# Optimization experiments

Hardware: AMD Instinct MI355X
Metric: run time of the kernel (lower is better)

## Reference

```python
import jax, jax.numpy as jnp
import numpy as np

H_DIM = 1024
N_HEADS = 16
HEAD_D = H_DIM // N_HEADS  # 64


def setup_inputs() -> dict:
    key = jax.random.key(0)
    ks = jax.random.split(key, 10)
    B, T, C = 2, 2048, H_DIM
    init = 1.0 / np.sqrt(C)  # lecun_normal-scale stand-in
    src = jax.random.normal(ks[0], (B, T, C), dtype=jnp.float32)
    mask = jnp.ones((B, T), dtype=jnp.float32)  # unused when causal
    Wq = jax.random.normal(ks[1], (C, H_DIM), dtype=jnp.float32) * init
    Wk = jax.random.normal(ks[2], (C, H_DIM), dtype=jnp.float32) * init
    Wv = jax.random.normal(ks[3], (C, H_DIM), dtype=jnp.float32) * init
    Wo = jax.random.normal(ks[4], (H_DIM, H_DIM), dtype=jnp.float32) * init
    bq = jnp.zeros((H_DIM,), jnp.float32)
    bk = jnp.zeros((H_DIM,), jnp.float32)
    bv = jnp.zeros((H_DIM,), jnp.float32)
    bo = jnp.zeros((H_DIM,), jnp.float32)
    return {"src": src, "mask": mask, "Wq": Wq, "bq": bq, "Wk": Wk, "bk": bk,
            "Wv": Wv, "bv": bv, "Wo": Wo, "bo": bo}


def reference(src, mask, Wq, bq, Wk, bk, Wv, bv, Wo, bo):
    # MaskedCausalAttention forward, deterministic=True (dropout = identity),
    # use_causal_mask=True.
    B, T, C = src.shape
    N, D = N_HEADS, HEAD_D
    # q,k,v: [B, N, T, D]
    q = (src @ Wq + bq).reshape(B, T, N, D).transpose(0, 2, 1, 3)
    k = (src @ Wk + bk).reshape(B, T, N, D).transpose(0, 2, 1, 3)
    v = (src @ Wv + bv).reshape(B, T, N, D).transpose(0, 2, 1, 3)
    # scores: [B, N, T, T]
    scores = jnp.einsum('bntd,bnsd->bnts', q, k) / jnp.sqrt(jnp.float32(D))
    causal = jnp.tril(jnp.ones((T, T), dtype=bool))[None, None]
    scores = jnp.where(causal, scores, -jnp.inf)
    probs = jax.nn.softmax(scores, axis=-1)
    attn = jnp.einsum('bnts,bnsd->bntd', probs, v)  # [B, N, T, D]
    attn = attn.transpose(0, 2, 1, 3).reshape(B, T, N * D)
    return attn @ Wo + bo
```

## Files before the change

### kernel.cpp

```cpp
#include <hip/hip_runtime.h>
#include <hip/hip_bf16.h>

typedef __hip_bfloat16 bf16;
typedef __attribute__((ext_vector_type(8))) short short8;
typedef __attribute__((ext_vector_type(4))) float f32x4;

#define BATCH 2
#define SEQ   2048
#define HDIM  1024
#define NHEAD 16
#define DHEAD 64
#define MROWS (BATCH*SEQ)

#define QSCALE 0.18033688f
#define EXP2F(x) __builtin_amdgcn_exp2f(x)

static __device__ __forceinline__ short f2bs(float x) {
    __hip_bfloat16 h = (__hip_bfloat16)x;
    return *reinterpret_cast<short*>(&h);
}
static __device__ __forceinline__ unsigned int pk2(float a, float b) {
    __hip_bfloat162 h = __float22bfloat162_rn(make_float2(a, b));
    return *reinterpret_cast<unsigned int*>(&h);
}

static __device__ __forceinline__ void gload16(const void* g, void* l) {
    __builtin_amdgcn_global_load_lds(
        (const __attribute__((address_space(1))) unsigned int*)g,
        (__attribute__((address_space(3))) unsigned int*)l, 16, 0, 0);
}

__global__ __launch_bounds__(256) void prep1(const float* __restrict__ src,
        const float* __restrict__ Wq, const float* __restrict__ Wk,
        const float* __restrict__ Wv,
        short* __restrict__ Sb, short* __restrict__ WqkT,
        short* __restrict__ WvT)
{
    __shared__ float t[64][65];
    const int bx = blockIdx.x, tid = threadIdx.x;
    if (bx < 4096) {
        int i = bx * 256 + tid;
        float4 v = ((const float4*)src)[i];
        ushort4 o;
        o.x = (unsigned short)f2bs(v.x);
        o.y = (unsigned short)f2bs(v.y);
        o.z = (unsigned short)f2bs(v.z);
        o.w = (unsigned short)f2bs(v.w);
        ((ushort4*)Sb)[i] = o;
        return;
    }
    const int tb = bx - 4096;
    const int wsel = tb >> 8;
    const float* W = (wsel == 0) ? Wq : (wsel == 1) ? Wk : Wv;
    short* dst = (wsel < 2) ? WqkT : WvT;
    const int roff = (wsel < 2) ? wsel * 1024 : 0;
    const int t8 = tb & 255;
    const int n0 = (t8 & 15) * 64, k0 = (t8 >> 4) * 64;
#pragma unroll
    for (int i = 0; i < 16; i++) {
        int idx = tid + i * 256, r = idx >> 6, c = idx & 63;
        t[r][c] = W[(size_t)(k0 + r) * HDIM + n0 + c];
    }
    __syncthreads();
#pragma unroll
    for (int i = 0; i < 16; i++) {
        int idx = tid + i * 256, c = idx >> 6, r = idx & 63;
        dst[(size_t)(roff + n0 + c) * HDIM + k0 + r] = f2bs(t[r][c]);
    }
}

__global__ __launch_bounds__(256) void gemm_qk(const short* __restrict__ A,
        const short* __restrict__ Bt,
        const float* __restrict__ bq, const float* __restrict__ bk,
        short* __restrict__ Qout, short* __restrict__ Kout)
{
    __shared__ short As[2][4 * 512];
    __shared__ short Bs[2][8 * 512];
    const int tid = threadIdx.x, lane = tid & 63, w = tid >> 6;
    const int quad = lane >> 4, l15 = lane & 15;
    const int m0 = blockIdx.y * 64, n0 = blockIdx.x * 128;
    const int wr = w >> 1, wc = w & 1;

    const short* gsrc[3];
    short* dst0[3];
    short* dst1[3];
#pragma unroll
    for (int i = 0; i < 3; i++) {
        int u = w * 3 + i;
        if (u < 4) {
            gsrc[i] = A + (size_t)(m0 + u * 16 + l15) * HDIM + quad * 8;
            dst0[i] = &As[0][u * 512];
            dst1[i] = &As[1][u * 512];
        } else {
            int c = u - 4;
            gsrc[i] = Bt + (size_t)(n0 + c * 16 + l15) * HDIM + quad * 8;
            dst0[i] = &Bs[0][c * 512];
            dst1[i] = &Bs[1][c * 512];
        }
    }

    f32x4 acc[2][4];
#pragma unroll
    for (int i = 0; i < 2; i++)
#pragma unroll
        for (int j = 0; j < 4; j++) acc[i][j] = (f32x4){0.f, 0.f, 0.f, 0.f};

#pragma unroll
    for (int i = 0; i < 3; i++) { gload16(gsrc[i], dst0[i]); gsrc[i] += 32; }
    __syncthreads();

    for (int kk = 0; kk < 32; ++kk) {
        const int cur = kk & 1;
        if (kk < 31) {
#pragma unroll
            for (int i = 0; i < 3; i++) {
                gload16(gsrc[i], cur ? dst0[i] : dst1[i]);
                gsrc[i] += 32;
            }
        }
        short8 af[2], bfr[4];
#pragma unroll
        for (int mi = 0; mi < 2; mi++)
            af[mi] = *(const short8*)&As[cur][(wr * 2 + mi) * 512 + lane * 8];
#pragma unroll
        for (int ni = 0; ni < 4; ni++)
            bfr[ni] = *(const short8*)&Bs[cur][(wc * 4 + ni) * 512 + lane * 8];
#pragma unroll
        for (int mi = 0; mi < 2; mi++)
#pragma unroll
            for (int ni = 0; ni < 4; ni++)
                acc[mi][ni] = __builtin_amdgcn_mfma_f32_16x16x32_bf16(
                                  af[mi], bfr[ni], acc[mi][ni], 0, 0, 0);
        __syncthreads();
    }

    const int region = n0 >> 10;
    const float* bias = region ? bk : bq;
    const float oscale = region ? 1.0f : QSCALE;
    short* C = region ? Kout : Qout;

#pragma unroll
    for (int mi = 0; mi < 2; mi++) {
        int mB = m0 + (wr * 2 + mi) * 16 + quad * 4;
#pragma unroll
        for (int ni = 0; ni < 4; ni++) {
            int nl = (n0 + (wc * 4 + ni) * 16 + l15) & 1023;
            float bb = bias[nl];
#pragma unroll
            for (int r = 0; r < 4; r++)
                C[(size_t)(mB + r) * HDIM + nl] =
                    f2bs((acc[mi][ni][r] + bb) * oscale);
        }
    }
}

__global__ __launch_bounds__(256) void gemm_v(const short* __restrict__ A,
        const short* __restrict__ Bt, const float* __restrict__ bv,
        short* __restrict__ Vtout)
{
    __shared__ short As[2][4 * 512];
    __shared__ short Bs[2][8 * 512];
    const int tid = threadIdx.x, lane = tid & 63, w = tid >> 6;
    const int quad = lane >> 4, l15 = lane & 15;
    const int m0 = blockIdx.y * 64, n0 = blockIdx.x * 128;
    const int wr = w >> 1, wc = w & 1;

    const short* gsrc[3];
    short* dst0[3];
    short* dst1[3];
#pragma unroll
    for (int i = 0; i < 3; i++) {
        int u = w * 3 + i;
        if (u < 4) {
            gsrc[i] = A + (size_t)(m0 + u * 16 + l15) * HDIM + quad * 8;
            dst0[i] = &As[0][u * 512];
            dst1[i] = &As[1][u * 512];
        } else {
            int c = u - 4;
            gsrc[i] = Bt + (size_t)(n0 + c * 16 + l15) * HDIM + quad * 8;
            dst0[i] = &Bs[0][c * 512];
            dst1[i] = &Bs[1][c * 512];
        }
    }

    f32x4 acc[2][4];
#pragma unroll
    for (int i = 0; i < 2; i++)
#pragma unroll
        for (int j = 0; j < 4; j++) acc[i][j] = (f32x4){0.f, 0.f, 0.f, 0.f};

#pragma unroll
    for (int i = 0; i < 3; i++) { gload16(gsrc[i], dst0[i]); gsrc[i] += 32; }
    __syncthreads();

    for (int kk = 0; kk < 32; ++kk) {
        const int cur = kk & 1;
        if (kk < 31) {
#pragma unroll
            for (int i = 0; i < 3; i++) {
                gload16(gsrc[i], cur ? dst0[i] : dst1[i]);
                gsrc[i] += 32;
            }
        }
        short8 af[2], bfr[4];
#pragma unroll
        for (int mi = 0; mi < 2; mi++)
            af[mi] = *(const short8*)&As[cur][(wr * 2 + mi) * 512 + lane * 8];
#pragma unroll
        for (int ni = 0; ni < 4; ni++)
            bfr[ni] = *(const short8*)&Bs[cur][(wc * 4 + ni) * 512 + lane * 8];
#pragma unroll
        for (int mi = 0; mi < 2; mi++)
#pragma unroll
            for (int ni = 0; ni < 4; ni++)
                acc[mi][ni] = __builtin_amdgcn_mfma_f32_16x16x32_bf16(
                                  af[mi], bfr[ni], acc[mi][ni], 0, 0, 0);
        __syncthreads();
    }

#pragma unroll
    for (int mi = 0; mi < 2; mi++) {
        int mB = m0 + (wr * 2 + mi) * 16 + quad * 4;
        int bb = mB >> 11, t = mB & 2047;
#pragma unroll
        for (int ni = 0; ni < 4; ni++) {
            int n = n0 + (wc * 4 + ni) * 16 + l15;
            int h = n >> 6, d = n & 63;
            float bvv = bv[n];
            size_t base = ((size_t)((bb * NHEAD + h) * DHEAD + d)) * SEQ + t;
            ushort4 pk;
            pk.x = (unsigned short)f2bs(acc[mi][ni][0] + bvv);
            pk.y = (unsigned short)f2bs(acc[mi][ni][1] + bvv);
            pk.z = (unsigned short)f2bs(acc[mi][ni][2] + bvv);
            pk.w = (unsigned short)f2bs(acc[mi][ni][3] + bvv);
            *(ushort4*)(Vtout + base) = pk;
        }
    }
}

__global__ __launch_bounds__(256) void gemm_o(const short* __restrict__ A,
        const short* __restrict__ Bt, const float* __restrict__ bo,
        float* __restrict__ Out)
{
    __shared__ short As[2][4 * 512];
    __shared__ short Bs[2][8 * 512];
    const int tid = threadIdx.x, lane = tid & 63, w = tid >> 6;
    const int quad = lane >> 4, l15 = lane & 15;
    const int m0 = blockIdx.y * 64, n0 = blockIdx.x * 128;
    const int wr = w >> 1, wc = w & 1;

    const short* gsrc[3];
    short* dst0[3];
    short* dst1[3];
#pragma unroll
    for (int i = 0; i < 3; i++) {
        int u = w * 3 + i;
        if (u < 4) {
            gsrc[i] = A + (size_t)(m0 + u * 16 + l15) * HDIM + quad * 8;
            dst0[i] = &As[0][u * 512];
            dst1[i] = &As[1][u * 512];
        } else {
            int c = u - 4;
            gsrc[i] = Bt + (size_t)(n0 + c * 16 + l15) * HDIM + quad * 8;
            dst0[i] = &Bs[0][c * 512];
            dst1[i] = &Bs[1][c * 512];
        }
    }

    f32x4 acc[2][4];
#pragma unroll
    for (int i = 0; i < 2; i++)
#pragma unroll
        for (int j = 0; j < 4; j++) acc[i][j] = (f32x4){0.f, 0.f, 0.f, 0.f};

#pragma unroll
    for (int i = 0; i < 3; i++) { gload16(gsrc[i], dst0[i]); gsrc[i] += 32; }
    __syncthreads();

    for (int kk = 0; kk < 32; ++kk) {
        const int cur = kk & 1;
        if (kk < 31) {
#pragma unroll
            for (int i = 0; i < 3; i++) {
                gload16(gsrc[i], cur ? dst0[i] : dst1[i]);
                gsrc[i] += 32;
            }
        }
        short8 af[2], bfr[4];
#pragma unroll
        for (int mi = 0; mi < 2; mi++)
            af[mi] = *(const short8*)&As[cur][(wr * 2 + mi) * 512 + lane * 8];
#pragma unroll
        for (int ni = 0; ni < 4; ni++)
            bfr[ni] = *(const short8*)&Bs[cur][(wc * 4 + ni) * 512 + lane * 8];
#pragma unroll
        for (int mi = 0; mi < 2; mi++)
#pragma unroll
            for (int ni = 0; ni < 4; ni++)
                acc[mi][ni] = __builtin_amdgcn_mfma_f32_16x16x32_bf16(
                                  af[mi], bfr[ni], acc[mi][ni], 0, 0, 0);
        __syncthreads();
    }

#pragma unroll
    for (int mi = 0; mi < 2; mi++) {
        int mB = m0 + (wr * 2 + mi) * 16 + quad * 4;
#pragma unroll
        for (int ni = 0; ni < 4; ni++) {
            int n = n0 + (wc * 4 + ni) * 16 + l15;
            float bb = bo[n];
#pragma unroll
            for (int r = 0; r < 4; r++)
                Out[(size_t)(mB + r) * HDIM + n] = acc[mi][ni][r] + bb;
        }
    }
}

__global__ __launch_bounds__(256) void attn_mfma(const short* __restrict__ Qb,
        const short* __restrict__ Kb, const short* __restrict__ Vt,
        short* __restrict__ Ab,
        const float* __restrict__ Wo, short* __restrict__ WoT)
{
    __shared__ short SMEM[12800];
    short* Ks = SMEM;
    short* Vs = SMEM + 4096;
    short* Ps = SMEM + 8192;
    const int tid = threadIdx.x, lane = tid & 63, w = tid >> 6;
    const int quad = lane >> 4, l15 = lane & 15;
    const int L = blockIdx.x;

    if (L >= 1024) {
        float* t = (float*)SMEM;
        const int bsel = L - 1024;
#pragma unroll
        for (int j = 0; j < 8; j++) {
            int t8 = bsel * 8 + j;
            int n0 = (t8 & 15) * 64, k0 = (t8 >> 4) * 64;
            __syncthreads();
#pragma unroll
            for (int i = 0; i < 16; i++) {
                int idx = tid + i * 256, r = idx >> 6, c = idx & 63;
                t[r * 65 + c] = Wo[(size_t)(k0 + r) * HDIM + n0 + c];
            }
            __syncthreads();
#pragma unroll
            for (int i = 0; i < 16; i++) {
                int idx = tid + i * 256, c = idx >> 6, r = idx & 63;
                WoT[(size_t)(n0 + c) * HDIM + k0 + r] = f2bs(t[r * 65 + c]);
            }
        }
        return;
    }

    const int pair = (L & 7) + 8 * ((L >> 3) & 3);
    const int strip = 31 - (L >> 5);
    const int b = pair >> 4, head = pair & 15;

    const short* Kbh = Kb + (size_t)b * SEQ * HDIM + head * DHEAD;
    const short* Vth = Vt + (size_t)(b * NHEAD + head) * DHEAD * SEQ;
    short* Pw = &Ps[w * 1152];

    const int qbase = strip * 64;
    const int qr = qbase + w * 16 + l15;

    const short* qptr = Qb + (size_t)(b * SEQ + qr) * HDIM + head * DHEAD + quad * 8;
    short8 bq0 = *(const short8*)qptr;
    short8 bq1 = *(const short8*)(qptr + 32);

    f32x4 o[4];
#pragma unroll
    for (int dt = 0; dt < 4; dt++) o[dt] = (f32x4){0.f, 0.f, 0.f, 0.f};
    float psum = 0.f;

    for (int it = 0; it <= strip; ++it) {
        const int s0 = it * 64;
#pragma unroll
        for (int i = 0; i < 4; i++) {
            int u = w * 4 + i;
            if (u < 8) {
                int t = u >> 1, h = u & 1;
                gload16(Kbh + (size_t)(s0 + t * 16 + l15) * HDIM + h * 32 + quad * 8,
                        &Ks[u * 512]);
            } else {
                int c = u - 8, dt = c >> 1, kh = c & 1;
                gload16(Vth + (size_t)(dt * 16 + l15) * SEQ + s0 + kh * 32 + quad * 8,
                        &Vs[c * 512]);
            }
        }
        __syncthreads();

        f32x4 sv[4];
#pragma unroll
        for (int t = 0; t < 4; t++) {
            sv[t] = (f32x4){0.f, 0.f, 0.f, 0.f};
            short8 k0 = *(const short8*)&Ks[(t * 2) * 512 + lane * 8];
            short8 k1 = *(const short8*)&Ks[(t * 2 + 1) * 512 + lane * 8];
            sv[t] = __builtin_amdgcn_mfma_f32_16x16x32_bf16(k0, bq0, sv[t], 0, 0, 0);
            sv[t] = __builtin_amdgcn_mfma_f32_16x16x32_bf16(k1, bq1, sv[t], 0, 0, 0);
        }

        float p[16];
        if (it == strip) {
#pragma unroll
            for (int t = 0; t < 4; t++)
#pragma unroll
                for (int r = 0; r < 4; r++) {
                    int key = s0 + t * 16 + quad * 4 + r;
                    p[t * 4 + r] = (key <= qr) ? EXP2F(sv[t][r]) : 0.f;
                }
        } else {
#pragma unroll
            for (int t = 0; t < 4; t++)
#pragma unroll
                for (int r = 0; r < 4; r++)
                    p[t * 4 + r] = EXP2F(sv[t][r]);
        }
#pragma unroll
        for (int i = 0; i < 16; i++) psum += p[i];

#pragma unroll
        for (int t = 0; t < 4; t++) {
            uint2 u2;
            u2.x = pk2(p[t * 4],     p[t * 4 + 1]);
            u2.y = pk2(p[t * 4 + 2], p[t * 4 + 3]);
            *(uint2*)&Pw[l15 * 72 + t * 16 + quad * 4] = u2;
        }
        short8 bp0 = *(const short8*)&Pw[l15 * 72 + quad * 8];
        short8 bp1 = *(const short8*)&Pw[l15 * 72 + 32 + quad * 8];

#pragma unroll
        for (int dt = 0; dt < 4; dt++) {
            short8 av0 = *(const short8*)&Vs[(dt * 2) * 512 + lane * 8];
            short8 av1 = *(const short8*)&Vs[(dt * 2 + 1) * 512 + lane * 8];
            o[dt] = __builtin_amdgcn_mfma_f32_16x16x32_bf16(av0, bp0, o[dt], 0, 0, 0);
            o[dt] = __builtin_amdgcn_mfma_f32_16x16x32_bf16(av1, bp1, o[dt], 0, 0, 0);
        }
        __syncthreads();
    }

    float lrow = psum + __shfl_xor(psum, 16);
    lrow += __shfl_xor(lrow, 32);
    const float inv = 1.f / lrow;

    const size_t obase = (size_t)(b * SEQ + qr) * HDIM + head * DHEAD;
#pragma unroll
    for (int dt = 0; dt < 4; dt++) {
        uint2 u2;
        u2.x = pk2(o[dt][0] * inv, o[dt][1] * inv);
        u2.y = pk2(o[dt][2] * inv, o[dt][3] * inv);
        *(uint2*)&Ab[obase + dt * 16 + quad * 4] = u2;
    }
}

extern "C" void kernel_launch(void* const* d_in, const int* in_sizes, int n_in,
                              void* d_out, int out_size, void* d_ws, size_t ws_size,
                              hipStream_t stream)
{
    const float* src = (const float*)d_in[0];
    const float* Wq = (const float*)d_in[2];
    const float* bq = (const float*)d_in[3];
    const float* Wk = (const float*)d_in[4];
    const float* bk = (const float*)d_in[5];
    const float* Wv = (const float*)d_in[6];
    const float* bv = (const float*)d_in[7];
    const float* Wo = (const float*)d_in[8];
    const float* bo = (const float*)d_in[9];
    float* out = (float*)d_out;

    short* Sb   = (short*)d_ws;
    short* Qb   = Sb + (size_t)MROWS * HDIM;
    short* Kb   = Qb + (size_t)MROWS * HDIM;
    short* Vt   = Kb + (size_t)MROWS * HDIM;
    short* slot = Vt + (size_t)MROWS * HDIM;
    short* WqkT = Vt;
    short* Ab   = Qb;

    dim3 blk(256);

    prep1<<<dim3(4096 + 768), blk, 0, stream>>>(src, Wq, Wk, Wv, Sb, WqkT, slot);

    gemm_qk<<<dim3(16, 64), blk, 0, stream>>>(Sb, WqkT, bq, bk, Qb, Kb);

    gemm_v<<<dim3(8, 64), blk, 0, stream>>>(Sb, slot, bv, Vt);

    attn_mfma<<<dim3(1024 + 32), blk, 0, stream>>>(Qb, Kb, Vt, Ab, Wo, slot);

    gemm_o<<<dim3(8, 64), blk, 0, stream>>>(Ab, slot, bo, out);
}
```

Measured before the change: 240.3 us.

## Fuse src bf16 conversion into a single QKV GEMM and move Wo transpose to prep

Removes the separate pass that converts src to bf16 and instead loads fp32 src directly in the GEMM, converting in registers before the LDS store. Merges the QK and V projection GEMMs into one launch over a 3072-wide concatenated weight with a larger 128x128 tile, and moves the Wo transpose out of the attention kernel into the weight prep kernel. This cuts a full read/write round trip of the activation and one launch, at the cost of more registers per thread (16 accumulators) and synchronous fp32 global loads in the GEMM loop.

Result: slower. 247.4 us (+3.0%).

```diff
diff --git a/kernel.cpp b/kernel.cpp
--- a/kernel.cpp
+++ b/kernel.cpp
@@ -30,31 +30,19 @@
         (__attribute__((address_space(3))) unsigned int*)l, 16, 0, 0);
 }
 
-__global__ __launch_bounds__(256) void prep1(const float* __restrict__ src,
-        const float* __restrict__ Wq, const float* __restrict__ Wk,
-        const float* __restrict__ Wv,
-        short* __restrict__ Sb, short* __restrict__ WqkT,
-        short* __restrict__ WvT)
+__global__ __launch_bounds__(256) void prep(const float* __restrict__ Wq,
+        const float* __restrict__ Wk, const float* __restrict__ Wv,
+        const float* __restrict__ Wo,
+        short* __restrict__ WqkvT, short* __restrict__ WoT)
 {
     __shared__ float t[64][65];
-    const int bx = blockIdx.x, tid = threadIdx.x;
-    if (bx < 4096) {
-        int i = bx * 256 + tid;
-        float4 v = ((const float4*)src)[i];
-        ushort4 o;
-        o.x = (unsigned short)f2bs(v.x);
-        o.y = (unsigned short)f2bs(v.y);
-        o.z = (unsigned short)f2bs(v.z);
-        o.w = (unsigned short)f2bs(v.w);
-        ((ushort4*)Sb)[i] = o;
-        return;
-    }
-    const int tb = bx - 4096;
-    const int wsel = tb >> 8;
-    const float* W = (wsel == 0) ? Wq : (wsel == 1) ? Wk : Wv;
-    short* dst = (wsel < 2) ? WqkT : WvT;
-    const int roff = (wsel < 2) ? wsel * 1024 : 0;
-    const int t8 = tb & 255;
+    const int tid = threadIdx.x;
+    const int wsel = blockIdx.x >> 8;
+    const float* W = (wsel == 0) ? Wq : (wsel == 1) ? Wk
+                    : (wsel == 2) ? Wv : Wo;
+    short* dst = (wsel < 3) ? WqkvT : WoT;
+    const int roff = (wsel < 3) ? wsel * 1024 : 0;
+    const int t8 = blockIdx.x & 255;
     const int n0 = (t8 & 15) * 64, k0 = (t8 >> 4) * 64;
 #pragma unroll
     for (int i = 0; i < 16; i++) {
@@ -69,10 +57,154 @@
     }
 }
 
-__global__ __launch_bounds__(256) void gemm_qk(const short* __restrict__ A,
+__global__ __launch_bounds__(256) void gemm_qkv(const float* __restrict__ src,
         const short* __restrict__ Bt,
         const float* __restrict__ bq, const float* __restrict__ bk,
-        short* __restrict__ Qout, short* __restrict__ Kout)
+        const float* __restrict__ bv,
+        short* __restrict__ Qout, short* __restrict__ Kout,
+        short* __restrict__ Vtout)
+{
+    __shared__ short As[2][8 * 512];
+    __shared__ short Bs[2][8 * 512];
+    const int tid = threadIdx.x, lane = tid & 63, w = tid >> 6;
+    const int quad = lane >> 4, l15 = lane & 15;
+    const int m0 = blockIdx.y * 128, n0 = blockIdx.x * 128;
+    const int wr = w >> 1, wc = w & 1;
+
+    const float* ag[2];
+    short* adst0[2];
+    short* adst1[2];
+#pragma unroll
+    for (int c = 0; c < 2; c++) {
+        int u = 2 * w + c;
+        ag[c] = src + (size_t)(m0 + u * 16 + l15) * HDIM + quad * 8;
+        adst0[c] = &As[0][u * 512 + lane * 8];
+        adst1[c] = &As[1][u * 512 + lane * 8];
+    }
+    const short* bg[2];
+    short* bdst0[2];
+    short* bdst1[2];
+#pragma unroll
+    for (int c = 0; c < 2; c++) {
+        int u = 2 * w + c;
+        bg[c] = Bt + (size_t)(n0 + u * 16 + l15) * HDIM + quad * 8;
+        bdst0[c] = &Bs[0][u * 512];
+        bdst1[c] = &Bs[1][u * 512];
+    }
+
+    f32x4 acc[4][4];
+#pragma unroll
+    for (int i = 0; i < 4; i++)
+#pragma unroll
+        for (int j = 0; j < 4; j++) acc[i][j] = (f32x4){0.f, 0.f, 0.f, 0.f};
+
+    {
+        float4 a4[2][2];
+#pragma unroll
+        for (int c = 0; c < 2; c++) {
+            a4[c][0] = *(const float4*)(ag[c]);
+            a4[c][1] = *(const float4*)(ag[c] + 4);
+            ag[c] += 32;
+            gload16(bg[c], bdst0[c]);
+            bg[c] += 32;
+        }
+#pragma unroll
+        for (int c = 0; c < 2; c++) {
+            uint4 u;
+            u.x = pk2(a4[c][0].x, a4[c][0].y);
+            u.y = pk2(a4[c][0].z, a4[c][0].w);
+            u.z = pk2(a4[c][1].x, a4[c][1].y);
+            u.w = pk2(a4[c][1].z, a4[c][1].w);
+            *(uint4*)adst0[c] = u;
+        }
+    }
+    __syncthreads();
+
+    for (int kk = 0; kk < 32; ++kk) {
+        const int cur = kk & 1;
+        float4 a4[2][2];
+        if (kk < 31) {
+#pragma unroll
+            for (int c = 0; c < 2; c++) {
+                a4[c][0] = *(const float4*)(ag[c]);
+                a4[c][1] = *(const float4*)(ag[c] + 4);
+                ag[c] += 32;
+                gload16(bg[c], cur ? bdst0[c] : bdst1[c]);
+                bg[c] += 32;
+            }
+        }
+
+        short8 af[4], bfr[4];
+#pragma unroll
+        for (int mi = 0; mi < 4; mi++)
+            af[mi] = *(const short8*)&As[cur][(wr * 4 + mi) * 512 + lane * 8];
+#pragma unroll
+        for (int ni = 0; ni < 4; ni++)
+            bfr[ni] = *(const short8*)&Bs[cur][(wc * 4 + ni) * 512 + lane * 8];
+#pragma unroll
+        for (int mi = 0; mi < 4; mi++)
+#pragma unroll
+            for (int ni = 0; ni < 4; ni++)
+                acc[mi][ni] = __builtin_amdgcn_mfma_f32_16x16x32_bf16(
+                                  af[mi], bfr[ni], acc[mi][ni], 0, 0, 0);
+
+        if (kk < 31) {
+#pragma unroll
+            for (int c = 0; c < 2; c++) {
+                uint4 u;
+                u.x = pk2(a4[c][0].x, a4[c][0].y);
+                u.y = pk2(a4[c][0].z, a4[c][0].w);
+                u.z = pk2(a4[c][1].x, a4[c][1].y);
+                u.w = pk2(a4[c][1].z, a4[c][1].w);
+                *(uint4*)(cur ? adst0[c] : adst1[c]) = u;
+            }
+        }
+        __syncthreads();
+    }
+
+    const int region = n0 >> 10;
+    const float* bias = (region == 0) ? bq : (region == 1) ? bk : bv;
+    const float oscale = (region == 0) ? QSCALE : 1.0f;
+
+    float bvv[4];
+    int nl4[4];
+#pragma unroll
+    for (int ni = 0; ni < 4; ni++) {
+        int n = n0 + (wc * 4 + ni) * 16 + l15;
+        nl4[ni] = n & 1023;
+        bvv[ni] = bias[nl4[ni]];
+    }
+
+#pragma unroll
+    for (int mi = 0; mi < 4; mi++) {
+        int mB = m0 + (wr * 4 + mi) * 16 + quad * 4;
+#pragma unroll
+        for (int ni = 0; ni < 4; ni++) {
+            int nl = nl4[ni];
+            if (region == 2) {
+                int bb = mB >> 11, t = mB & 2047;
+                int h = nl >> 6, d = nl & 63;
+                size_t base = ((size_t)((bb * NHEAD + h) * DHEAD + d)) * SEQ + t;
+                ushort4 pk;
+                pk.x = (unsigned short)f2bs(acc[mi][ni][0] + bvv[ni]);
+                pk.y = (unsigned short)f2bs(acc[mi][ni][1] + bvv[ni]);
+                pk.z = (unsigned short)f2bs(acc[mi][ni][2] + bvv[ni]);
+                pk.w = (unsigned short)f2bs(acc[mi][ni][3] + bvv[ni]);
+                *(ushort4*)(Vtout + base) = pk;
+            } else {
+                short* C = (region == 0) ? Qout : Kout;
+#pragma unroll
+                for (int r = 0; r < 4; r++)
+                    C[(size_t)(mB + r) * HDIM + nl] =
+                        f2bs((acc[mi][ni][r] + bvv[ni]) * oscale);
+            }
+        }
+    }
+}
+
+__global__ __launch_bounds__(256) void gemm_o(const short* __restrict__ A,
+        const short* __restrict__ Bt, const float* __restrict__ bo,
+        float* __restrict__ Out)
 {
     __shared__ short As[2][4 * 512];
     __shared__ short Bs[2][8 * 512];
@@ -134,174 +266,6 @@
         __syncthreads();
     }
 
-    const int region = n0 >> 10;
-    const float* bias = region ? bk : bq;
-    const float oscale = region ? 1.0f : QSCALE;
-    short* C = region ? Kout : Qout;
-
-#pragma unroll
-    for (int mi = 0; mi < 2; mi++) {
-        int mB = m0 + (wr * 2 + mi) * 16 + quad * 4;
-#pragma unroll
-        for (int ni = 0; ni < 4; ni++) {
-            int nl = (n0 + (wc * 4 + ni) * 16 + l15) & 1023;
-            float bb = bias[nl];
-#pragma unroll
-            for (int r = 0; r < 4; r++)
-                C[(size_t)(mB + r) * HDIM + nl] =
-                    f2bs((acc[mi][ni][r] + bb) * oscale);
-        }
-    }
-}
-
-__global__ __launch_bounds__(256) void gemm_v(const short* __restrict__ A,
-        const short* __restrict__ Bt, const float* __restrict__ bv,
-        short* __restrict__ Vtout)
-{
-    __shared__ short As[2][4 * 512];
-    __shared__ short Bs[2][8 * 512];
-    const int tid = threadIdx.x, lane = tid & 63, w = tid >> 6;
-    const int quad = lane >> 4, l15 = lane & 15;
-    const int m0 = blockIdx.y * 64, n0 = blockIdx.x * 128;
-    const int wr = w >> 1, wc = w & 1;
-
-    const short* gsrc[3];
-    short* dst0[3];
-    short* dst1[3];
-#pragma unroll
-    for (int i = 0; i < 3; i++) {
-        int u = w * 3 + i;
-        if (u < 4) {
-            gsrc[i] = A + (size_t)(m0 + u * 16 + l15) * HDIM + quad * 8;
-            dst0[i] = &As[0][u * 512];
-            dst1[i] = &As[1][u * 512];
-        } else {
-            int c = u - 4;
-            gsrc[i] = Bt + (size_t)(n0 + c * 16 + l15) * HDIM + quad * 8;
-            dst0[i] = &Bs[0][c * 512];
-            dst1[i] = &Bs[1][c * 512];
-        }
-    }
-
-    f32x4 acc[2][4];
-#pragma unroll
-    for (int i = 0; i < 2; i++)
-#pragma unroll
-        for (int j = 0; j < 4; j++) acc[i][j] = (f32x4){0.f, 0.f, 0.f, 0.f};
-
-#pragma unroll
-    for (int i = 0; i < 3; i++) { gload16(gsrc[i], dst0[i]); gsrc[i] += 32; }
-    __syncthreads();
-
-    for (int kk = 0; kk < 32; ++kk) {
-        const int cur = kk & 1;
-        if (kk < 31) {
-#pragma unroll
-            for (int i = 0; i < 3; i++) {
-                gload16(gsrc[i], cur ? dst0[i] : dst1[i]);
-                gsrc[i] += 32;
-            }
-        }
-        short8 af[2], bfr[4];
-#pragma unroll
-        for (int mi = 0; mi < 2; mi++)
-            af[mi] = *(const short8*)&As[cur][(wr * 2 + mi) * 512 + lane * 8];
-#pragma unroll
-        for (int ni = 0; ni < 4; ni++)
-            bfr[ni] = *(const short8*)&Bs[cur][(wc * 4 + ni) * 512 + lane * 8];
-#pragma unroll
-        for (int mi = 0; mi < 2; mi++)
-#pragma unroll
-            for (int ni = 0; ni < 4; ni++)
-                acc[mi][ni] = __builtin_amdgcn_mfma_f32_16x16x32_bf16(
-                                  af[mi], bfr[ni], acc[mi][ni], 0, 0, 0);
-        __syncthreads();
-    }
-
-#pragma unroll
-    for (int mi = 0; mi < 2; mi++) {
-        int mB = m0 + (wr * 2 + mi) * 16 + quad * 4;
-        int bb = mB >> 11, t = mB & 2047;
-#pragma unroll
-        for (int ni = 0; ni < 4; ni++) {
-            int n = n0 + (wc * 4 + ni) * 16 + l15;
-            int h = n >> 6, d = n & 63;
-            float bvv = bv[n];
-            size_t base = ((size_t)((bb * NHEAD + h) * DHEAD + d)) * SEQ + t;
-            ushort4 pk;
-            pk.x = (unsigned short)f2bs(acc[mi][ni][0] + bvv);
-            pk.y = (unsigned short)f2bs(acc[mi][ni][1] + bvv);
-            pk.z = (unsigned short)f2bs(acc[mi][ni][2] + bvv);
-            pk.w = (unsigned short)f2bs(acc[mi][ni][3] + bvv);
-            *(ushort4*)(Vtout + base) = pk;
-        }
-    }
-}
-
-__global__ __launch_bounds__(256) void gemm_o(const short* __restrict__ A,
-        const short* __restrict__ Bt, const float* __restrict__ bo,
-        float* __restrict__ Out)
-{
-    __shared__ short As[2][4 * 512];
-    __shared__ short Bs[2][8 * 512];
-    const int tid = threadIdx.x, lane = tid & 63, w = tid >> 6;
-    const int quad = lane >> 4, l15 = lane & 15;
-    const int m0 = blockIdx.y * 64, n0 = blockIdx.x * 128;
-    const int wr = w >> 1, wc = w & 1;
-
-    const short* gsrc[3];
-    short* dst0[3];
-    short* dst1[3];
-#pragma unroll
-    for (int i = 0; i < 3; i++) {
-        int u = w * 3 + i;
-        if (u < 4) {
-            gsrc[i] = A + (size_t)(m0 + u * 16 + l15) * HDIM + quad * 8;
-            dst0[i] = &As[0][u * 512];
-            dst1[i] = &As[1][u * 512];
-        } else {
-            int c = u - 4;
-            gsrc[i] = Bt + (size_t)(n0 + c * 16 + l15) * HDIM + quad * 8;
-            dst0[i] = &Bs[0][c * 512];
-            dst1[i] = &Bs[1][c * 512];
-        }
-    }
-
-    f32x4 acc[2][4];
-#pragma unroll
-    for (int i = 0; i < 2; i++)
-#pragma unroll
-        for (int j = 0; j < 4; j++) acc[i][j] = (f32x4){0.f, 0.f, 0.f, 0.f};
-
-#pragma unroll
-    for (int i = 0; i < 3; i++) { gload16(gsrc[i], dst0[i]); gsrc[i] += 32; }
-    __syncthreads();
-
-    for (int kk = 0; kk < 32; ++kk) {
-        const int cur = kk & 1;
-        if (kk < 31) {
-#pragma unroll
-            for (int i = 0; i < 3; i++) {
-                gload16(gsrc[i], cur ? dst0[i] : dst1[i]);
-                gsrc[i] += 32;
-            }
-        }
-        short8 af[2], bfr[4];
-#pragma unroll
-        for (int mi = 0; mi < 2; mi++)
-            af[mi] = *(const short8*)&As[cur][(wr * 2 + mi) * 512 + lane * 8];
-#pragma unroll
-        for (int ni = 0; ni < 4; ni++)
-            bfr[ni] = *(const short8*)&Bs[cur][(wc * 4 + ni) * 512 + lane * 8];
-#pragma unroll
-        for (int mi = 0; mi < 2; mi++)
-#pragma unroll
-            for (int ni = 0; ni < 4; ni++)
-                acc[mi][ni] = __builtin_amdgcn_mfma_f32_16x16x32_bf16(
-                                  af[mi], bfr[ni], acc[mi][ni], 0, 0, 0);
-        __syncthreads();
-    }
-
 #pragma unroll
     for (int mi = 0; mi < 2; mi++) {
         int mB = m0 + (wr * 2 + mi) * 16 + quad * 4;
@@ -318,8 +282,7 @@
 
 __global__ __launch_bounds__(256) void attn_mfma(const short* __restrict__ Qb,
         const short* __restrict__ Kb, const short* __restrict__ Vt,
-        short* __restrict__ Ab,
-        const float* __restrict__ Wo, short* __restrict__ WoT)
+        short* __restrict__ Ab)
 {
     __shared__ short SMEM[12800];
     short* Ks = SMEM;
@@ -328,29 +291,6 @@
     const int tid = threadIdx.x, lane = tid & 63, w = tid >> 6;
     const int quad = lane >> 4, l15 = lane & 15;
     const int L = blockIdx.x;
-
-    if (L >= 1024) {
-        float* t = (float*)SMEM;
-        const int bsel = L - 1024;
-#pragma unroll
-        for (int j = 0; j < 8; j++) {
-            int t8 = bsel * 8 + j;
-            int n0 = (t8 & 15) * 64, k0 = (t8 >> 4) * 64;
-            __syncthreads();
-#pragma unroll
-            for (int i = 0; i < 16; i++) {
-                int idx = tid + i * 256, r = idx >> 6, c = idx & 63;
-                t[r * 65 + c] = Wo[(size_t)(k0 + r) * HDIM + n0 + c];
-            }
-            __syncthreads();
-#pragma unroll
-            for (int i = 0; i < 16; i++) {
-                int idx = tid + i * 256, c = idx >> 6, r = idx & 63;
-                WoT[(size_t)(n0 + c) * HDIM + k0 + r] = f2bs(t[r * 65 + c]);
-            }
-        }
-        return;
-    }
 
     const int pair = (L & 7) + 8 * ((L >> 3) & 3);
     const int strip = 31 - (L >> 5);
@@ -467,23 +407,21 @@
     const float* bo = (const float*)d_in[9];
     float* out = (float*)d_out;
 
-    short* Sb   = (short*)d_ws;
-    short* Qb   = Sb + (size_t)MROWS * HDIM;
-    short* Kb   = Qb + (size_t)MROWS * HDIM;
-    short* Vt   = Kb + (size_t)MROWS * HDIM;
-    short* slot = Vt + (size_t)MROWS * HDIM;
-    short* WqkT = Vt;
-    short* Ab   = Qb;
+    short* WqkvT = (short*)d_ws;
+    short* WoT   = WqkvT + (size_t)3 * HDIM * HDIM;
+    short* Qb    = WoT   + (size_t)HDIM * HDIM;
+    short* Kb    = Qb + (size_t)MROWS * HDIM;
+    short* Vt    = Kb + (size_t)MROWS * HDIM;
+    short* Ab    = Qb;
 
     dim3 blk(256);
 
-    prep1<<<dim3(4096 + 768), blk, 0, stream>>>(src, Wq, Wk, Wv, Sb, WqkT, slot);
-
-    gemm_qk<<<dim3(16, 64), blk, 0, stream>>>(Sb, WqkT, bq, bk, Qb, Kb);
-
-    gemm_v<<<dim3(8, 64), blk, 0, stream>>>(Sb, slot, bv, Vt);
-
-    attn_mfma<<<dim3(1024 + 32), blk, 0, stream>>>(Qb, Kb, Vt, Ab, Wo, slot);
-
-    gemm_o<<<dim3(8, 64), blk, 0, stream>>>(Ab, slot, bo, out);
-}
+    prep<<<dim3(1024), blk, 0, stream>>>(Wq, Wk, Wv, Wo, WqkvT, WoT);
+
+    gemm_qkv<<<dim3(24, 32), blk, 0, stream>>>(src, WqkvT, bq, bk, bv,
+                                               Qb, Kb, Vt);
+
+    attn_mfma<<<dim3(1024), blk, 0, stream>>>(Qb, Kb, Vt, Ab);
+
+    gemm_o<<<dim3(8, 64), blk, 0, stream>>>(Ab, WoT, bo, out);
+}
```

## Enlarge GEMM K-step to 64 and QK tile to 128x128 with single-buffered LDS

Applied to the files above, without the earlier changes.

All three projection GEMMs now load a 64-wide K slice per iteration (16 iterations instead of 32), which halves the number of barriers per K. They drop the double-buffered prefetch in favour of a load-sync-compute pattern. The QK GEMM also grows its block tile from 64x128 to 128x128, with 16 accumulators per wave and half as many blocks, to improve operand reuse. In exchange, global loads no longer overlap with MFMA work inside a block, and the larger QK tile uses more registers and LDS, which may lower occupancy.

Measured after the change: 226.9 us. -5.6%, faster.

```diff
diff --git a/kernel.cpp b/kernel.cpp
--- a/kernel.cpp
+++ b/kernel.cpp
@@ -74,28 +74,106 @@
         const float* __restrict__ bq, const float* __restrict__ bk,
         short* __restrict__ Qout, short* __restrict__ Kout)
 {
-    __shared__ short As[2][4 * 512];
-    __shared__ short Bs[2][8 * 512];
+    __shared__ short As[16 * 512];
+    __shared__ short Bs[16 * 512];
+    const int tid = threadIdx.x, lane = tid & 63, w = tid >> 6;
+    const int quad = lane >> 4, l15 = lane & 15;
+    const int m0 = blockIdx.y * 128, n0 = blockIdx.x * 128;
+    const int wr = w >> 1, wc = w & 1;
+
+    const short* gsrc[8];
+    short* ldst[8];
+#pragma unroll
+    for (int i = 0; i < 8; i++) {
+        int u = w * 8 + i;
+        if (u < 16) {
+            int mi = u >> 1, kh = u & 1;
+            gsrc[i] = A + (size_t)(m0 + mi * 16 + l15) * HDIM + kh * 32 + quad * 8;
+            ldst[i] = &As[u * 512];
+        } else {
+            int v = u - 16, ni = v >> 1, kh = v & 1;
+            gsrc[i] = Bt + (size_t)(n0 + ni * 16 + l15) * HDIM + kh * 32 + quad * 8;
+            ldst[i] = &Bs[v * 512];
+        }
+    }
+
+    f32x4 acc[4][4];
+#pragma unroll
+    for (int i = 0; i < 4; i++)
+#pragma unroll
+        for (int j = 0; j < 4; j++) acc[i][j] = (f32x4){0.f, 0.f, 0.f, 0.f};
+
+    for (int kk = 0; kk < 16; ++kk) {
+        if (kk) __syncthreads();
+#pragma unroll
+        for (int i = 0; i < 8; i++) {
+            gload16(gsrc[i], ldst[i]);
+            gsrc[i] += 64;
+        }
+        __syncthreads();
+
+#pragma unroll
+        for (int kh = 0; kh < 2; kh++) {
+            short8 af[4], bfr[4];
+#pragma unroll
+            for (int mi = 0; mi < 4; mi++)
+                af[mi] = *(const short8*)&As[((wr * 4 + mi) * 2 + kh) * 512 + lane * 8];
+#pragma unroll
+            for (int ni = 0; ni < 4; ni++)
+                bfr[ni] = *(const short8*)&Bs[((wc * 4 + ni) * 2 + kh) * 512 + lane * 8];
+#pragma unroll
+            for (int mi = 0; mi < 4; mi++)
+#pragma unroll
+                for (int ni = 0; ni < 4; ni++)
+                    acc[mi][ni] = __builtin_amdgcn_mfma_f32_16x16x32_bf16(
+                                      af[mi], bfr[ni], acc[mi][ni], 0, 0, 0);
+        }
+    }
+
+    const int region = n0 >> 10;
+    const float* bias = region ? bk : bq;
+    const float oscale = region ? 1.0f : QSCALE;
+    short* C = region ? Kout : Qout;
+
+#pragma unroll
+    for (int mi = 0; mi < 4; mi++) {
+        int mB = m0 + (wr * 4 + mi) * 16 + quad * 4;
+#pragma unroll
+        for (int ni = 0; ni < 4; ni++) {
+            int nl = (n0 + (wc * 4 + ni) * 16 + l15) & 1023;
+            float bb = bias[nl];
+#pragma unroll
+            for (int r = 0; r < 4; r++)
+                C[(size_t)(mB + r) * HDIM + nl] =
+                    f2bs((acc[mi][ni][r] + bb) * oscale);
+        }
+    }
+}
+
+__global__ __launch_bounds__(256) void gemm_v(const short* __restrict__ A,
+        const short* __restrict__ Bt, const float* __restrict__ bv,
+        short* __restrict__ Vtout)
+{
+    __shared__ short As[8 * 512];
+    __shared__ short Bs[16 * 512];
     const int tid = threadIdx.x, lane = tid & 63, w = tid >> 6;
     const int quad = lane >> 4, l15 = lane & 15;
     const int m0 = blockIdx.y * 64, n0 = blockIdx.x * 128;
     const int wr = w >> 1, wc = w & 1;
 
-    const short* gsrc[3];
-    short* dst0[3];
-    short* dst1[3];
-#pragma unroll
-    for (int i = 0; i < 3; i++) {
-        int u = w * 3 + i;
-        if (u < 4) {
-            gsrc[i] = A + (size_t)(m0 + u * 16 + l15) * HDIM + quad * 8;
-            dst0[i] = &As[0][u * 512];
-            dst1[i] = &As[1][u * 512];
+    const short* gsrc[6];
+    short* ldst[6];
+#pragma unroll
+    for (int i = 0; i < 6; i++) {
+        int u = w * 6 + i;
+        if (u < 8) {
+            int mi = u >> 1, kh = u & 1;
+            gsrc[i] = A + (size_t)(m0 + mi * 16 + l15) * HDIM + kh * 32 + quad * 8;
+            ldst[i] = &As[u * 512];
         } else {
-            int c = u - 4;
-            gsrc[i] = Bt + (size_t)(n0 + c * 16 + l15) * HDIM + quad * 8;
-            dst0[i] = &Bs[0][c * 512];
-            dst1[i] = &Bs[1][c * 512];
+            int v = u - 8, ni = v >> 1, kh = v & 1;
+            gsrc[i] = Bt + (size_t)(n0 + ni * 16 + l15) * HDIM + kh * 32 + quad * 8;
+            ldst[i] = &Bs[v * 512];
         }
     }
 
@@ -105,117 +183,31 @@
 #pragma unroll
         for (int j = 0; j < 4; j++) acc[i][j] = (f32x4){0.f, 0.f, 0.f, 0.f};
 
-#pragma unroll
-    for (int i = 0; i < 3; i++) { gload16(gsrc[i], dst0[i]); gsrc[i] += 32; }
-    __syncthreads();
-
-    for (int kk = 0; kk < 32; ++kk) {
-        const int cur = kk & 1;
-        if (kk < 31) {
-#pragma unroll
-            for (int i = 0; i < 3; i++) {
-                gload16(gsrc[i], cur ? dst0[i] : dst1[i]);
-                gsrc[i] += 32;
-            }
-        }
-        short8 af[2], bfr[4];
-#pragma unroll
-        for (int mi = 0; mi < 2; mi++)
-            af[mi] = *(const short8*)&As[cur][(wr * 2 + mi) * 512 + lane * 8];
-#pragma unroll
-        for (int ni = 0; ni < 4; ni++)
-            bfr[ni] = *(const short8*)&Bs[cur][(wc * 4 + ni) * 512 + lane * 8];
-#pragma unroll
-        for (int mi = 0; mi < 2; mi++)
+    for (int kk = 0; kk < 16; ++kk) {
+        if (kk) __syncthreads();
+#pragma unroll
+        for (int i = 0; i < 6; i++) {
+            gload16(gsrc[i], ldst[i]);
+            gsrc[i] += 64;
+        }
+        __syncthreads();
+
+#pragma unroll
+        for (int kh = 0; kh < 2; kh++) {
+            short8 af[2], bfr[4];
+#pragma unroll
+            for (int mi = 0; mi < 2; mi++)
+                af[mi] = *(const short8*)&As[((wr * 2 + mi) * 2 + kh) * 512 + lane * 8];
 #pragma unroll
             for (int ni = 0; ni < 4; ni++)
-                acc[mi][ni] = __builtin_amdgcn_mfma_f32_16x16x32_bf16(
-                                  af[mi], bfr[ni], acc[mi][ni], 0, 0, 0);
-        __syncthreads();
-    }
-
-    const int region = n0 >> 10;
-    const float* bias = region ? bk : bq;
-    const float oscale = region ? 1.0f : QSCALE;
-    short* C = region ? Kout : Qout;
-
-#pragma unroll
-    for (int mi = 0; mi < 2; mi++) {
-        int mB = m0 + (wr * 2 + mi) * 16 + quad * 4;
-#pragma unroll
-        for (int ni = 0; ni < 4; ni++) {
-            int nl = (n0 + (wc * 4 + ni) * 16 + l15) & 1023;
-            float bb = bias[nl];
-#pragma unroll
-            for (int r = 0; r < 4; r++)
-                C[(size_t)(mB + r) * HDIM + nl] =
-                    f2bs((acc[mi][ni][r] + bb) * oscale);
-        }
-    }
-}
-
-__global__ __launch_bounds__(256) void gemm_v(const short* __restrict__ A,
-        const short* __restrict__ Bt, const float* __restrict__ bv,
-        short* __restrict__ Vtout)
-{
-    __shared__ short As[2][4 * 512];
-    __shared__ short Bs[2][8 * 512];
-    const int tid = threadIdx.x, lane = tid & 63, w = tid >> 6;
-    const int quad = lane >> 4, l15 = lane & 15;
-    const int m0 = blockIdx.y * 64, n0 = blockIdx.x * 128;
-    const int wr = w >> 1, wc = w & 1;
-
-    const short* gsrc[3];
-    short* dst0[3];
-    short* dst1[3];
-#pragma unroll
-    for (int i = 0; i < 3; i++) {
-        int u = w * 3 + i;
-        if (u < 4) {
-            gsrc[i] = A + (size_t)(m0 + u * 16 + l15) * HDIM + quad * 8;
-            dst0[i] = &As[0][u * 512];
-            dst1[i] = &As[1][u * 512];
-        } else {
-            int c = u - 4;
-            gsrc[i] = Bt + (size_t)(n0 + c * 16 + l15) * HDIM + quad * 8;
-            dst0[i] = &Bs[0][c * 512];
-            dst1[i] = &Bs[1][c * 512];
-        }
-    }
-
-    f32x4 acc[2][4];
-#pragma unroll
-    for (int i = 0; i < 2; i++)
-#pragma unroll
-        for (int j = 0; j < 4; j++) acc[i][j] = (f32x4){0.f, 0.f, 0.f, 0.f};
-
-#pragma unroll
-    for (int i = 0; i < 3; i++) { gload16(gsrc[i], dst0[i]); gsrc[i] += 32; }
-    __syncthreads();
-
-    for (int kk = 0; kk < 32; ++kk) {
-        const int cur = kk & 1;
-        if (kk < 31) {
-#pragma unroll
-            for (int i = 0; i < 3; i++) {
-                gload16(gsrc[i], cur ? dst0[i] : dst1[i]);
-                gsrc[i] += 32;
-            }
-        }
-        short8 af[2], bfr[4];
-#pragma unroll
-        for (int mi = 0; mi < 2; mi++)
-            af[mi] = *(const short8*)&As[cur][(wr * 2 + mi) * 512 + lane * 8];
-#pragma unroll
-        for (int ni = 0; ni < 4; ni++)
-            bfr[ni] = *(const short8*)&Bs[cur][(wc * 4 + ni) * 512 + lane * 8];
-#pragma unroll
-        for (int mi = 0; mi < 2; mi++)
-#pragma unroll
-            for (int ni = 0; ni < 4; ni++)
-                acc[mi][ni] = __builtin_amdgcn_mfma_f32_16x16x32_bf16(
-                                  af[mi], bfr[ni], acc[mi][ni], 0, 0, 0);
-        __syncthreads();
+                bfr[ni] = *(const short8*)&Bs[((wc * 4 + ni) * 2 + kh) * 512 + lane * 8];
+#pragma unroll
+            for (int mi = 0; mi < 2; mi++)
+#pragma unroll
+                for (int ni = 0; ni < 4; ni++)
+                    acc[mi][ni] = __builtin_amdgcn_mfma_f32_16x16x32_bf16(
+                                      af[mi], bfr[ni], acc[mi][ni], 0, 0, 0);
+        }
     }
 
 #pragma unroll
@@ -242,28 +234,26 @@
         const short* __restrict__ Bt, const float* __restrict__ bo,
         float* __restrict__ Out)
 {
-    __shared__ short As[2][4 * 512];
-    __shared__ short Bs[2][8 * 512];
+    __shared__ short As[8 * 512];
+    __shared__ short Bs[16 * 512];
     const int tid = threadIdx.x, lane = tid & 63, w = tid >> 6;
     const int quad = lane >> 4, l15 = lane & 15;
     const int m0 = blockIdx.y * 64, n0 = blockIdx.x * 128;
     const int wr = w >> 1, wc = w & 1;
 
-    const short* gsrc[3];
-    short* dst0[3];
-    short* dst1[3];
-#pragma unroll
-    for (int i = 0; i < 3; i++) {
-        int u = w * 3 + i;
-        if (u < 4) {
-            gsrc[i] = A + (size_t)(m0 + u * 16 + l15) * HDIM + quad * 8;
-            dst0[i] = &As[0][u * 512];
-            dst1[i] = &As[1][u * 512];
+    const short* gsrc[6];
+    short* ldst[6];
+#pragma unroll
+    for (int i = 0; i < 6; i++) {
+        int u = w * 6 + i;
+        if (u < 8) {
+            int mi = u >> 1, kh = u & 1;
+            gsrc[i] = A + (size_t)(m0 + mi * 16 + l15) * HDIM + kh * 32 + quad * 8;
+            ldst[i] = &As[u * 512];
         } else {
-            int c = u - 4;
-            gsrc[i] = Bt + (size_t)(n0 + c * 16 + l15) * HDIM + quad * 8;
-            dst0[i] = &Bs[0][c * 512];
-            dst1[i] = &Bs[1][c * 512];
+            int v = u - 8, ni = v >> 1, kh = v & 1;
+            gsrc[i] = Bt + (size_t)(n0 + ni * 16 + l15) * HDIM + kh * 32 + quad * 8;
+            ldst[i] = &Bs[v * 512];
         }
     }
 
@@ -273,33 +263,31 @@
 #pragma unroll
         for (int j = 0; j < 4; j++) acc[i][j] = (f32x4){0.f, 0.f, 0.f, 0.f};
 
-#pragma unroll
-    for (int i = 0; i < 3; i++) { gload16(gsrc[i], dst0[i]); gsrc[i] += 32; }
-    __syncthreads();
-
-    for (int kk = 0; kk < 32; ++kk) {
-        const int cur = kk & 1;
-        if (kk < 31) {
-#pragma unroll
-            for (int i = 0; i < 3; i++) {
-                gload16(gsrc[i], cur ? dst0[i] : dst1[i]);
-                gsrc[i] += 32;
-            }
-        }
-        short8 af[2], bfr[4];
-#pragma unroll
-        for (int mi = 0; mi < 2; mi++)
-            af[mi] = *(const short8*)&As[cur][(wr * 2 + mi) * 512 + lane * 8];
-#pragma unroll
-        for (int ni = 0; ni < 4; ni++)
-            bfr[ni] = *(const short8*)&Bs[cur][(wc * 4 + ni) * 512 + lane * 8];
-#pragma unroll
-        for (int mi = 0; mi < 2; mi++)
+    for (int kk = 0; kk < 16; ++kk) {
+        if (kk) __syncthreads();
+#pragma unroll
+        for (int i = 0; i < 6; i++) {
+            gload16(gsrc[i], ldst[i]);
+            gsrc[i] += 64;
+        }
+        __syncthreads();
+
+#pragma unroll
+        for (int kh = 0; kh < 2; kh++) {
+            short8 af[2], bfr[4];
+#pragma unroll
+            for (int mi = 0; mi < 2; mi++)
+                af[mi] = *(const short8*)&As[((wr * 2 + mi) * 2 + kh) * 512 + lane * 8];
 #pragma unroll
             for (int ni = 0; ni < 4; ni++)
-                acc[mi][ni] = __builtin_amdgcn_mfma_f32_16x16x32_bf16(
-                                  af[mi], bfr[ni], acc[mi][ni], 0, 0, 0);
-        __syncthreads();
+                bfr[ni] = *(const short8*)&Bs[((wc * 4 + ni) * 2 + kh) * 512 + lane * 8];
+#pragma unroll
+            for (int mi = 0; mi < 2; mi++)
+#pragma unroll
+                for (int ni = 0; ni < 4; ni++)
+                    acc[mi][ni] = __builtin_amdgcn_mfma_f32_16x16x32_bf16(
+                                      af[mi], bfr[ni], acc[mi][ni], 0, 0, 0);
+        }
     }
 
 #pragma unroll
@@ -479,7 +467,7 @@
 
     prep1<<<dim3(4096 + 768), blk, 0, stream>>>(src, Wq, Wk, Wv, Sb, WqkT, slot);
 
-    gemm_qk<<<dim3(16, 64), blk, 0, stream>>>(Sb, WqkT, bq, bk, Qb, Kb);
+    gemm_qk<<<dim3(16, 32), blk, 0, stream>>>(Sb, WqkT, bq, bk, Qb, Kb);
 
     gemm_v<<<dim3(8, 64), blk, 0, stream>>>(Sb, slot, bv, Vt);
 
```
